# Kernel tuning notes

Measured on AMD Instinct MI355X. Metric: run time of the kernel, lower is better.

## Reference

```python
import jax, jax.numpy as jnp
import numpy as np
from functools import partial

B, T, P, W = 32, 4096, 512, 128
NMEL, FILT, PDIM, K = 80, 256, 64, 9
PAD = (K - 1) // 2  # original uses (kernel[0][0]-1)//2 for both convs
EPS = 1e-5


def setup_inputs() -> dict:
    key = jax.random.key(0)
    ks = jax.random.split(key, 8)
    inp = {}
    inp["mask"] = jnp.zeros((B, P), dtype=bool)
    inp["mels"] = jax.random.normal(ks[0], (B, T, NMEL), dtype=jnp.float32)
    inp["mel_mask"] = jnp.zeros((B, T), dtype=bool)
    # uniform segments: 8 frames per phone (sum == T), 4 phones per word (sum == P)
    inp["durations"] = jnp.full((B, P), T // P, dtype=jnp.int32)
    inp["word_phone_len"] = jnp.full((B, W), P // W, dtype=jnp.int32)
    s1 = 1.0 / np.sqrt(NMEL * K)
    s2 = 1.0 / np.sqrt(FILT * K)
    s3 = 1.0 / np.sqrt(FILT)
    inp["conv1_w"] = jax.random.normal(ks[1], (FILT, NMEL, K), dtype=jnp.float32) * s1
    inp["conv1_b"] = jnp.zeros((FILT,), dtype=jnp.float32)
    inp["ln1_g"] = jnp.ones((FILT,), dtype=jnp.float32)
    inp["ln1_b"] = jnp.zeros((FILT,), dtype=jnp.float32)
    inp["conv2_w"] = jax.random.normal(ks[2], (FILT, FILT, K), dtype=jnp.float32) * s2
    inp["conv2_b"] = jnp.zeros((FILT,), dtype=jnp.float32)
    inp["ln2_g"] = jnp.ones((FILT,), dtype=jnp.float32)
    inp["ln2_b"] = jnp.zeros((FILT,), dtype=jnp.float32)
    inp["w1"] = jax.random.normal(ks[3], (FILT, FILT), dtype=jnp.float32) * s3
    inp["b1"] = jnp.zeros((FILT,), dtype=jnp.float32)
    inp["w2"] = jax.random.normal(ks[4], (FILT, PDIM), dtype=jnp.float32) * s3
    inp["b2"] = jnp.zeros((PDIM,), dtype=jnp.float32)
    return inp


def conv1d(x, w, b):
    # x: [B, T, Cin], w: [Cout, Cin, K] -> [B, T, Cout]
    y = jax.lax.conv_general_dilated(x.transpose(0, 2, 1), w, (1,), [(PAD, PAD)])
    return y.transpose(0, 2, 1) + b


def layernorm(x, g, b):
    m = jnp.mean(x, axis=-1, keepdims=True)
    v = jnp.mean(jnp.square(x - m), axis=-1, keepdims=True)
    return (x - m) * jax.lax.rsqrt(v + EPS) * g + b


def seg_mean(feat, lens, n_seg):
    # feat: [L, D], lens: [S] -> [n_seg, D] segment means
    bounds = jnp.cumsum(lens)
    ids = jnp.searchsorted(bounds, jnp.arange(feat.shape[0]), side="right")
    s = jax.ops.segment_sum(feat, ids, num_segments=n_seg)
    cnt = jnp.maximum(lens, 1).astype(feat.dtype)
    return s / cnt[:, None]


def expand_words(word_emb, wlens, n_out):
    # word_emb: [W, D]; scatter each word embedding across its phones -> [n_out, D]
    bounds = jnp.cumsum(wlens)
    wid = jnp.searchsorted(bounds, jnp.arange(n_out), side="right")
    return word_emb[jnp.clip(wid, 0, word_emb.shape[0] - 1)]


def reference(mask, mels, mel_mask, durations, word_phone_len,
              conv1_w, conv1_b, ln1_g, ln1_b, conv2_w, conv2_b, ln2_g, ln2_b,
              w1, b1, w2, b2):
    x = conv1d(mels, conv1_w, conv1_b)
    x = layernorm(jax.nn.relu(x), ln1_g, ln1_b)
    x = conv1d(x, conv2_w, conv2_b)
    x = layernorm(jax.nn.relu(x), ln2_g, ln2_b)  # [B, T, FILT]
    # token-wise (phone) mean pool over mel frames
    x = jax.vmap(partial(seg_mean, n_seg=P))(x, durations)  # [B, P, FILT]
    # word-level mean pool over phones
    x = jax.vmap(partial(seg_mean, n_seg=W))(x, word_phone_len)  # [B, W, FILT]
    x = jax.nn.relu(x @ w1 + b1)
    x = jax.nn.relu(x @ w2 + b2)  # [B, W, PDIM]
    # expand word embeddings back to phone level
    x = jax.vmap(partial(expand_words, n_out=P))(x, word_phone_len)  # [B, P, PDIM]
    x = jnp.where(mask[..., None], 0.0, x)
    return x
```

## Files before the change

### kernel.cpp

```cpp
#include <hip/hip_runtime.h>
#include <hip/hip_fp16.h>
#include <stdint.h>

#define B_ 32
#define T_ 4096
#define P_ 512
#define W_ 128
#define NMEL 80
#define FILT 256
#define PDIM 64
#define KW 9
#define TP8 (T_ + 8)
#define MSTR 104
#define YSTR 264
#define EPS 1e-5f

typedef unsigned short u16;
typedef __attribute__((ext_vector_type(8))) short short8;
typedef __attribute__((ext_vector_type(4))) float f32x4;

typedef const __attribute__((address_space(1))) uint32_t* gptr_t;
typedef __attribute__((address_space(3))) uint32_t* lptr_t;

__device__ __forceinline__ u16 f2h(float v){ return __half_as_ushort(__float2half(v)); }

#define MFMA16(accv, av, bv) \
  asm volatile("v_mfma_f32_16x16x32_f16 %0, %1, %2, %0" : "+v"(accv) : "v"(av), "v"(bv))

#define STAGE16K(gbase, lbase) { \
    __builtin_amdgcn_global_load_lds((gptr_t)((gbase) + (wave<<10) + (lane<<4)), \
                                     (lptr_t)((lbase) + (wave<<10)), 16, 0, 0); \
    __builtin_amdgcn_global_load_lds((gptr_t)((gbase) + 8192 + (wave<<10) + (lane<<4)), \
                                     (lptr_t)((lbase) + 8192 + (wave<<10)), 16, 0, 0); \
  }

__global__ void pack_w(const float* __restrict__ w1, const float* __restrict__ w2,
                       u16* __restrict__ Wp1, u16* __restrict__ Wp2){
  int i = blockIdx.x * 256 + threadIdx.x;
  const int N1 = KW * 12 * FILT;
  const int N2 = KW * 32 * FILT;
  if (i < N1){
    int tap = i / (12*FILT); int r = i - tap*12*FILT; int kg = r / FILT; int co = r - kg*FILT;
    short8 v;
    #pragma unroll
    for (int e=0;e<8;e++){
      int ci = kg*8 + e;
      float x = (ci < NMEL) ? w1[(co*NMEL + ci)*KW + tap] : 0.f;
      v[e] = (short)f2h(x);
    }
    *(short8*)(Wp1 + (size_t)i*8) = v;
  } else if (i < N1 + N2){
    int j = i - N1;
    int tap = j / (32*FILT); int r = j - tap*32*FILT; int kg = r / FILT; int co = r - kg*FILT;
    short8 v;
    #pragma unroll
    for (int e=0;e<8;e++){
      int ci = kg*8 + e;
      v[e] = (short)f2h(w2[(co*FILT + ci)*KW + tap]);
    }
    *(short8*)(Wp2 + (size_t)j*8) = v;
  }
}

__global__ void prep_mels(const float* __restrict__ mels, u16* __restrict__ melsPad){
  int idx = blockIdx.x * 256 + threadIdx.x;
  if (idx >= B_*TP8*13) return;
  int ch = idx % 13; int r = idx / 13; int row = r % TP8; int b = r / TP8;
  int t = row - 4;
  short8 v = (short8){0,0,0,0,0,0,0,0};
  if (t >= 0 && t < T_ && ch < 10){
    const float* src = mels + ((size_t)b*T_ + t)*NMEL + ch*8;
    const f32x4 f0 = *(const f32x4*)src;
    const f32x4 f1 = *(const f32x4*)(src+4);
    #pragma unroll
    for (int j=0;j<4;j++){ v[j]=(short)f2h(f0[j]); v[4+j]=(short)f2h(f1[j]); }
  }
  *(short8*)(melsPad + (size_t)idx*8) = v;
}

__global__ void prep_seg(const int* __restrict__ dur, const int* __restrict__ wpl,
                         int* __restrict__ wcum,
                         int* __restrict__ pid, int* __restrict__ wid,
                         u16* __restrict__ y1Pad){
  int b = blockIdx.x; int tid = threadIdx.x;
  __shared__ int dc[P_];
  __shared__ int wc[W_];
  for (int p=tid; p<P_; p+=256) dc[p] = dur[b*P_+p];
  if (tid < W_) wc[tid] = wpl[b*W_+tid];
  __syncthreads();
  if (tid == 0){ int run=0; for (int p=0;p<P_;p++){ run += dc[p]; dc[p]=run; } }
  if (tid == 64){ int run=0; for (int w=0;w<W_;w++){ run += wc[w]; wc[w]=run; wcum[b*W_+w]=run; } }
  __syncthreads();
  for (int t=tid; t<T_; t+=256){
    int lo=0, hi=P_;
    while (lo < hi){ int mid=(lo+hi)>>1; if (dc[mid] > t) hi=mid; else lo=mid+1; }
    pid[b*T_+t] = lo;
  }
  for (int p=tid; p<P_; p+=256){
    int lo=0, hi=W_;
    while (lo < hi){ int mid=(lo+hi)>>1; if (wc[mid] > p) hi=mid; else lo=mid+1; }
    wid[b*P_+p] = min(lo, W_-1);
  }
  for (int i=tid; i<8*YSTR; i+=256){
    int rr = i / YSTR; int cc = i - rr*YSTR;
    int row = (rr < 4) ? rr : (T_ + rr);
    y1Pad[((size_t)b*TP8 + row)*YSTR + cc] = 0;
  }
}

__global__ __launch_bounds__(512, 6) void conv1_k(
    const u16* __restrict__ melsPad, const u16* __restrict__ Wp1,
    const float* __restrict__ bias, const float* __restrict__ lng,
    const float* __restrict__ lnb, u16* __restrict__ y1Pad){
  __shared__ __align__(16) u16 sA[8192];
  __shared__ __align__(16) u16 sR[2*8192];
  const int tid = threadIdx.x;
  const int wave = tid >> 6, lane = tid & 63, lo = lane & 15, hi = lane >> 4;
  const int b = blockIdx.y, t0 = blockIdx.x * 64;

  float bcol[2], gcol[2], btcol[2];
  #pragma unroll
  for (int n=0;n<2;n++){
    int c = wave*32 + n*16 + lo;
    bcol[n]=bias[c]; gcol[n]=lng[c]; btcol[n]=lnb[c];
  }

  {
    const char* gA = (const char*)(melsPad + ((size_t)b*TP8 + t0)*MSTR);
    #pragma unroll
    for (int it=0; it<2; ++it)
      __builtin_amdgcn_global_load_lds((gptr_t)(gA + it*8192 + (wave<<10) + (lane<<4)),
                                       (lptr_t)((char*)sA + it*8192 + (wave<<10)), 16, 0, 0);
  }
  const char* gW = (const char*)Wp1;
  char* ring = (char*)sR;
  STAGE16K(gW, ring)
  __syncthreads();

  f32x4 acc[4][2];
  #pragma unroll
  for (int m=0;m<4;m++)
    #pragma unroll
    for (int n=0;n<2;n++) acc[m][n] = (f32x4){0.f,0.f,0.f,0.f};

#define C1_IT(cc, WN) { \
    __builtin_amdgcn_s_barrier(); \
    __builtin_amdgcn_sched_barrier(0); \
    if ((cc)+1 < 27) STAGE16K(gW + (size_t)((cc)+1)*16384, ring + ((((cc)+1)&1)<<14)) \
    asm volatile("s_waitcnt vmcnt(" #WN ")" ::: "memory"); \
    __builtin_amdgcn_sched_barrier(0); \
    const int tap_=(cc)/3, s_=(cc)%3; \
    const u16* bufB = (const u16*)(ring + (((cc)&1)<<14)); \
    short8 av[4], wv[2]; \
    _Pragma("unroll") for (int m=0;m<4;m++) \
      av[m] = *(const short8*)(sA + (m*16 + lo + tap_)*MSTR + s_*32 + hi*8); \
    _Pragma("unroll") for (int n=0;n<2;n++) \
      wv[n] = *(const short8*)(bufB + (hi*256 + wave*32 + n*16 + lo)*8); \
    asm volatile("s_waitcnt lgkmcnt(0)" ::: "memory"); \
    __builtin_amdgcn_sched_barrier(0); \
    __builtin_amdgcn_s_setprio(1); \
    _Pragma("unroll") for (int m=0;m<4;m++) \
      _Pragma("unroll") for (int n=0;n<2;n++) \
        MFMA16(acc[m][n], av[m], wv[n]); \
    __builtin_amdgcn_s_setprio(0); \
  }

  #pragma unroll 1
  for (int cc=0; cc<26; ++cc) C1_IT(cc, 2)
  C1_IT(26, 0)

  asm volatile("s_nop 7\n\ts_nop 7" :: );
  __syncthreads();

  float* sred  = (float*)sR;
  float* sred2 = sred + 512;
  float* smean = sred2 + 512;
  float* srstd = smean + 64;

  #pragma unroll
  for (int m=0;m<4;m++){
    #pragma unroll
    for (int jj=0;jj<4;jj++){
      float s=0.f, q=0.f;
      #pragma unroll
      for (int n=0;n<2;n++){
        float v = fmaxf(acc[m][n][jj] + bcol[n], 0.f);
        s += v; q += v*v;
      }
      #pragma unroll
      for (int off=1; off<16; off<<=1){ s += __shfl_xor(s, off); q += __shfl_xor(q, off); }
      if (lo == 0){ int r = m*16 + hi*4 + jj; sred[r*8+wave] = s; sred2[r*8+wave] = q; }
    }
  }
  __syncthreads();
  if (tid < 64){
    float ss=0.f, qq=0.f;
    #pragma unroll
    for (int w2=0; w2<8; w2++){ ss += sred[tid*8+w2]; qq += sred2[tid*8+w2]; }
    float mean = ss * (1.f/FILT);
    float var  = qq * (1.f/FILT) - mean*mean;
    smean[tid] = mean;
    srstd[tid] = rsqrtf(fmaxf(var, 0.f) + EPS);
  }
  __syncthreads();
  #pragma unroll
  for (int m=0;m<4;m++){
    #pragma unroll
    for (int jj=0;jj<4;jj++){
      int r = m*16 + hi*4 + jj;
      float mn = smean[r], rs = srstd[r];
      #pragma unroll
      for (int n=0;n<2;n++){
        float v = fmaxf(acc[m][n][jj] + bcol[n], 0.f);
        float o = (v - mn)*rs*gcol[n] + btcol[n];
        y1Pad[((size_t)b*TP8 + 4 + t0 + r)*YSTR + wave*32 + n*16 + lo] = f2h(o);
      }
    }
  }
}

__global__ __launch_bounds__(512, 4) void conv2_k(
    const u16* __restrict__ y1Pad, const u16* __restrict__ Wp2,
    const float* __restrict__ bias, const float* __restrict__ lng,
    const float* __restrict__ lnb, const int* __restrict__ pid,
    float* __restrict__ ps){
  __shared__ __align__(16) u16 sA[20480];
  __shared__ __align__(16) u16 sR[2*8192];
  __shared__ int pidT[64];
  const int tid = threadIdx.x;
  const int wave = tid >> 6, lane = tid & 63, lo = lane & 15, hi = lane >> 4;
  const int b = blockIdx.y, t0 = blockIdx.x * 64;

  float bcol[2], gcol[2], btcol[2];
  #pragma unroll
  for (int n=0;n<2;n++){
    int c = wave*32 + n*16 + lo;
    bcol[n]=bias[c]; gcol[n]=lng[c]; btcol[n]=lnb[c];
  }
  if (tid < 64) pidT[tid] = pid[b*T_ + t0 + tid];

  {
    const char* gA = (const char*)(y1Pad + ((size_t)b*TP8 + t0)*YSTR);
    #pragma unroll
    for (int it=0; it<5; ++it)
      __builtin_amdgcn_global_load_lds((gptr_t)(gA + it*8192 + (wave<<10) + (lane<<4)),
                                       (lptr_t)((char*)sA + it*8192 + (wave<<10)), 16, 0, 0);
  }
  const char* gW = (const char*)Wp2;
  char* ring = (char*)sR;
  STAGE16K(gW, ring)
  __syncthreads();

  f32x4 acc[4][2];
  #pragma unroll
  for (int m=0;m<4;m++)
    #pragma unroll
    for (int n=0;n<2;n++) acc[m][n] = (f32x4){0.f,0.f,0.f,0.f};

#define C2_IT(cc, WN) { \
    __builtin_amdgcn_s_barrier(); \
    __builtin_amdgcn_sched_barrier(0); \
    if ((cc)+1 < 72) STAGE16K(gW + (size_t)((cc)+1)*16384, ring + ((((cc)+1)&1)<<14)) \
    asm volatile("s_waitcnt vmcnt(" #WN ")" ::: "memory"); \
    __builtin_amdgcn_sched_barrier(0); \
    const int tap_=(cc)>>3, sg_=(cc)&7; \
    const u16* bufB = (const u16*)(ring + (((cc)&1)<<14)); \
    short8 av[4], wv[2]; \
    _Pragma("unroll") for (int m=0;m<4;m++) \
      av[m] = *(const short8*)(sA + (m*16 + lo + tap_)*YSTR + sg_*32 + hi*8); \
    _Pragma("unroll") for (int n=0;n<2;n++) \
      wv[n] = *(const short8*)(bufB + (hi*256 + wave*32 + n*16 + lo)*8); \
    asm volatile("s_waitcnt lgkmcnt(0)" ::: "memory"); \
    __builtin_amdgcn_sched_barrier(0); \
    __builtin_amdgcn_s_setprio(1); \
    _Pragma("unroll") for (int m=0;m<4;m++) \
      _Pragma("unroll") for (int n=0;n<2;n++) \
        MFMA16(acc[m][n], av[m], wv[n]); \
    __builtin_amdgcn_s_setprio(0); \
  }

  #pragma unroll 1
  for (int cc=0; cc<71; ++cc) C2_IT(cc, 2)
  C2_IT(71, 0)

  asm volatile("s_nop 7\n\ts_nop 7" :: );
  __syncthreads();

  float* sred  = (float*)sR;
  float* sred2 = sred + 512;
  float* smean = sred2 + 512;
  float* srstd = smean + 64;

  #pragma unroll
  for (int m=0;m<4;m++){
    #pragma unroll
    for (int jj=0;jj<4;jj++){
      float s=0.f, q=0.f;
      #pragma unroll
      for (int n=0;n<2;n++){
        float v = fmaxf(acc[m][n][jj] + bcol[n], 0.f);
        s += v; q += v*v;
      }
      #pragma unroll
      for (int off=1; off<16; off<<=1){ s += __shfl_xor(s, off); q += __shfl_xor(q, off); }
      if (lo == 0){ int r = m*16 + hi*4 + jj; sred[r*8+wave] = s; sred2[r*8+wave] = q; }
    }
  }
  __syncthreads();
  if (tid < 64){
    float ss=0.f, qq=0.f;
    #pragma unroll
    for (int w2=0; w2<8; w2++){ ss += sred[tid*8+w2]; qq += sred2[tid*8+w2]; }
    float mean = ss * (1.f/FILT);
    float var  = qq * (1.f/FILT) - mean*mean;
    smean[tid] = mean;
    srstd[tid] = rsqrtf(fmaxf(var, 0.f) + EPS);
  }
  __syncthreads();

  #pragma unroll
  for (int m=0;m<4;m++){
    int rbase = m*16 + hi*4;
    int p0v = pidT[rbase], p3v = pidT[rbase+3];
    int fold = (p0v == p3v);
    float mn[4], rs[4];
    #pragma unroll
    for (int jj=0;jj<4;jj++){ int r = rbase+jj; mn[jj]=smean[r]; rs[jj]=srstd[r]; }
    #pragma unroll
    for (int n=0;n<2;n++){
      int c = wave*32 + n*16 + lo;
      float o[4];
      #pragma unroll
      for (int jj=0;jj<4;jj++){
        float v = fmaxf(acc[m][n][jj] + bcol[n], 0.f);
        o[jj] = (v - mn[jj])*rs[jj]*gcol[n] + btcol[n];
      }
      float s4 = fold ? (o[0]+o[1]+o[2]+o[3]) : 0.f;
      float sp = __shfl_xor(s4, 16);
      int   pp = __shfl_xor(p0v, 16);
      int   fp = __shfl_xor(fold, 16);
      float* base = ps + (size_t)b*P_*FILT;
      if (fold){
        if (p0v < P_){
          if (fp && pp == p0v){
            if ((hi & 1) == 0) atomicAdd(base + (size_t)p0v*FILT + c, s4 + sp);
          } else {
            atomicAdd(base + (size_t)p0v*FILT + c, s4);
          }
        }
      } else {
        #pragma unroll
        for (int jj=0;jj<4;jj++){
          int pj = pidT[rbase+jj];
          if (pj < P_) atomicAdd(base + (size_t)pj*FILT + c, o[jj]);
        }
      }
    }
  }
}

#define WPB 8
__global__ __launch_bounds__(256) void word_k(
    const float* __restrict__ ps, const int* __restrict__ dur,
    const int* __restrict__ wcum, const int* __restrict__ wpl,
    const float* __restrict__ w1, const float* __restrict__ b1,
    const float* __restrict__ w2, const float* __restrict__ b2,
    float* __restrict__ wemb){
  int b = blockIdx.y, wg = blockIdx.x * WPB, tid = threadIdx.x;
  __shared__ float wvS[WPB][FILT];
  __shared__ float h1S[WPB][FILT];
  #pragma unroll
  for (int k=0;k<WPB;k++){
    int w = wg + k;
    int p1 = wcum[b*W_ + w]; int p0 = (w == 0) ? 0 : wcum[b*W_ + w - 1];
    if (p1 > P_) p1 = P_;
    int len = wpl[b*W_ + w];
    float a = 0.f;
    for (int p = p0; p < p1; ++p){
      int d = dur[b*P_ + p]; d = d < 1 ? 1 : d;
      a += ps[((size_t)(b*P_ + p))*FILT + tid] / (float)d;
    }
    wvS[k][tid] = a / (float)(len < 1 ? 1 : len);
  }
  __syncthreads();
  float acc[WPB];
  #pragma unroll
  for (int k=0;k<WPB;k++) acc[k] = b1[tid];
  for (int i=0;i<FILT;i++){
    float wcol = w1[i*FILT + tid];
    #pragma unroll
    for (int k=0;k<WPB;k++) acc[k] += wvS[k][i] * wcol;
  }
  #pragma unroll
  for (int k=0;k<WPB;k++) h1S[k][tid] = fmaxf(acc[k], 0.f);
  __syncthreads();
  int c = tid & 63, kq = tid >> 6;
  #pragma unroll
  for (int kk=kq; kk<WPB; kk+=4){
    float u = b2[c];
    for (int i=0;i<FILT;i++) u += h1S[kk][i] * w2[i*PDIM + c];
    wemb[((size_t)(b*W_ + wg + kk))*PDIM + c] = fmaxf(u, 0.f);
  }
}

__global__ void expand_k(const float* __restrict__ wemb, const int* __restrict__ wid,
                         const unsigned char* __restrict__ mask, float* __restrict__ out){
  int idx = blockIdx.x * 256 + threadIdx.x;
  if (idx >= B_*P_*16) return;
  int q = idx & 15; int p = (idx >> 4) & 511; int bb = idx >> 13;
  int w = wid[bb*P_ + p];
  f32x4 v = *(const f32x4*)(wemb + ((size_t)(bb*W_ + w))*PDIM + q*4);
  if (mask[bb*P_ + p]) v = (f32x4){0.f,0.f,0.f,0.f};
  *(f32x4*)(out + (size_t)idx*4) = v;
}

extern "C" void kernel_launch(void* const* d_in, const int* in_sizes, int n_in,
                              void* d_out, int out_size, void* d_ws, size_t ws_size,
                              hipStream_t stream) {
  const unsigned char* mask = (const unsigned char*)d_in[0];
  const float* mels = (const float*)d_in[1];
  const int*   dur  = (const int*)d_in[3];
  const int*   wpl  = (const int*)d_in[4];
  const float* c1w  = (const float*)d_in[5];
  const float* c1b  = (const float*)d_in[6];
  const float* l1g  = (const float*)d_in[7];
  const float* l1b  = (const float*)d_in[8];
  const float* c2w  = (const float*)d_in[9];
  const float* c2b  = (const float*)d_in[10];
  const float* l2g  = (const float*)d_in[11];
  const float* l2b  = (const float*)d_in[12];
  const float* w1   = (const float*)d_in[13];
  const float* b1   = (const float*)d_in[14];
  const float* w2   = (const float*)d_in[15];
  const float* b2   = (const float*)d_in[16];

  char* ws = (char*)d_ws;
  size_t off = 0;
  auto alloc = [&](size_t bytes){ void* p = ws + off; off += (bytes + 255) & ~(size_t)255; return p; };
  u16* melsPad = (u16*)alloc((size_t)B_*TP8*MSTR*2 + 16384);
  u16* y1Pad   = (u16*)alloc((size_t)B_*TP8*YSTR*2 + 16384);
  u16* Wp1     = (u16*)alloc((size_t)KW*12*FILT*8*2);
  u16* Wp2     = (u16*)alloc((size_t)KW*32*FILT*8*2 + 16384);
  int* wcum    = (int*)alloc((size_t)B_*W_*4);
  int* pid     = (int*)alloc((size_t)B_*T_*4);
  int* wid     = (int*)alloc((size_t)B_*P_*4);
  float* psum  = (float*)alloc((size_t)B_*P_*FILT*4);
  float* wemb  = (float*)alloc((size_t)B_*W_*PDIM*4);

  hipMemsetAsync(psum, 0, (size_t)B_*P_*FILT*4, stream);
  pack_w<<<(KW*12*FILT + KW*32*FILT + 255)/256, 256, 0, stream>>>(c1w, c2w, Wp1, Wp2);
  prep_mels<<<(B_*TP8*13 + 255)/256, 256, 0, stream>>>(mels, melsPad);
  prep_seg<<<B_, 256, 0, stream>>>(dur, wpl, wcum, pid, wid, y1Pad);
  conv1_k<<<dim3(T_/64, B_), 512, 0, stream>>>(melsPad, Wp1, c1b, l1g, l1b, y1Pad);
  conv2_k<<<dim3(T_/64, B_), 512, 0, stream>>>(y1Pad, Wp2, c2b, l2g, l2b, pid, psum);
  word_k<<<dim3(W_/WPB, B_), 256, 0, stream>>>(psum, dur, wcum, wpl, w1, b1, w2, b2, wemb);
  expand_k<<<(B_*P_*16 + 255)/256, 256, 0, stream>>>(wemb, wid, mask, (float*)d_out);
}
```

Before: 382.8 us.

## Retile conv kernels to 128-row blocks with 32x32 MFMA and register-streamed weights

Both convolution kernels now process 128 time rows per block with 4 waves, each wave owning 64 output channels and computing with 32x32x16 MFMA tiles instead of 16x16x32. Weights are no longer staged through an LDS ring with barriers. Each lane loads them directly from global memory into registers and prefetches one chunk ahead, which removes the per-iteration block barrier. The larger per-wave tile is meant to raise MFMA density and weight reuse, at the cost of more accumulator registers and LDS per block, which lowers occupancy. Padding of the workspace buffers is enlarged to cover the bigger input tile loads.

```diff
diff --git a/kernel.cpp b/kernel.cpp
--- a/kernel.cpp
+++ b/kernel.cpp
@@ -18,21 +18,15 @@
 typedef unsigned short u16;
 typedef __attribute__((ext_vector_type(8))) short short8;
 typedef __attribute__((ext_vector_type(4))) float f32x4;
+typedef __attribute__((ext_vector_type(16))) float f32x16;
 
 typedef const __attribute__((address_space(1))) uint32_t* gptr_t;
 typedef __attribute__((address_space(3))) uint32_t* lptr_t;
 
 __device__ __forceinline__ u16 f2h(float v){ return __half_as_ushort(__float2half(v)); }
 
-#define MFMA16(accv, av, bv) \
-  asm volatile("v_mfma_f32_16x16x32_f16 %0, %1, %2, %0" : "+v"(accv) : "v"(av), "v"(bv))
-
-#define STAGE16K(gbase, lbase) { \
-    __builtin_amdgcn_global_load_lds((gptr_t)((gbase) + (wave<<10) + (lane<<4)), \
-                                     (lptr_t)((lbase) + (wave<<10)), 16, 0, 0); \
-    __builtin_amdgcn_global_load_lds((gptr_t)((gbase) + 8192 + (wave<<10) + (lane<<4)), \
-                                     (lptr_t)((lbase) + 8192 + (wave<<10)), 16, 0, 0); \
-  }
+#define MFMA32(accv, av, bv) \
+  asm volatile("v_mfma_f32_32x32x16_f16 %0, %1, %2, %0" : "+v"(accv) : "v"(av), "v"(bv))
 
 __global__ void pack_w(const float* __restrict__ w1, const float* __restrict__ w2,
                        u16* __restrict__ Wp1, u16* __restrict__ Wp2){
@@ -108,209 +102,213 @@
   }
 }
 
-__global__ __launch_bounds__(512, 6) void conv1_k(
+__global__ __launch_bounds__(256, 2) void conv1_k(
     const u16* __restrict__ melsPad, const u16* __restrict__ Wp1,
     const float* __restrict__ bias, const float* __restrict__ lng,
     const float* __restrict__ lnb, u16* __restrict__ y1Pad){
-  __shared__ __align__(16) u16 sA[8192];
-  __shared__ __align__(16) u16 sR[2*8192];
+  __shared__ __align__(16) u16 sA[14144];
+  __shared__ float sred[512], sred2[512], smean[128], srstd[128];
   const int tid = threadIdx.x;
-  const int wave = tid >> 6, lane = tid & 63, lo = lane & 15, hi = lane >> 4;
-  const int b = blockIdx.y, t0 = blockIdx.x * 64;
+  const int cg = tid >> 6, lane = tid & 63, l31 = lane & 31, h = lane >> 5;
+  const int b = blockIdx.y, t0 = blockIdx.x * 128;
 
   float bcol[2], gcol[2], btcol[2];
   #pragma unroll
   for (int n=0;n<2;n++){
-    int c = wave*32 + n*16 + lo;
+    int c = cg*64 + n*32 + l31;
     bcol[n]=bias[c]; gcol[n]=lng[c]; btcol[n]=lnb[c];
   }
 
   {
     const char* gA = (const char*)(melsPad + ((size_t)b*TP8 + t0)*MSTR);
     #pragma unroll
-    for (int it=0; it<2; ++it)
-      __builtin_amdgcn_global_load_lds((gptr_t)(gA + it*8192 + (wave<<10) + (lane<<4)),
-                                       (lptr_t)((char*)sA + it*8192 + (wave<<10)), 16, 0, 0);
-  }
-  const char* gW = (const char*)Wp1;
-  char* ring = (char*)sR;
-  STAGE16K(gW, ring)
-  __syncthreads();
-
-  f32x4 acc[4][2];
-  #pragma unroll
-  for (int m=0;m<4;m++)
-    #pragma unroll
-    for (int n=0;n<2;n++) acc[m][n] = (f32x4){0.f,0.f,0.f,0.f};
-
-#define C1_IT(cc, WN) { \
-    __builtin_amdgcn_s_barrier(); \
-    __builtin_amdgcn_sched_barrier(0); \
-    if ((cc)+1 < 27) STAGE16K(gW + (size_t)((cc)+1)*16384, ring + ((((cc)+1)&1)<<14)) \
-    asm volatile("s_waitcnt vmcnt(" #WN ")" ::: "memory"); \
-    __builtin_amdgcn_sched_barrier(0); \
-    const int tap_=(cc)/3, s_=(cc)%3; \
-    const u16* bufB = (const u16*)(ring + (((cc)&1)<<14)); \
-    short8 av[4], wv[2]; \
-    _Pragma("unroll") for (int m=0;m<4;m++) \
-      av[m] = *(const short8*)(sA + (m*16 + lo + tap_)*MSTR + s_*32 + hi*8); \
-    _Pragma("unroll") for (int n=0;n<2;n++) \
-      wv[n] = *(const short8*)(bufB + (hi*256 + wave*32 + n*16 + lo)*8); \
-    asm volatile("s_waitcnt lgkmcnt(0)" ::: "memory"); \
-    __builtin_amdgcn_sched_barrier(0); \
-    __builtin_amdgcn_s_setprio(1); \
-    _Pragma("unroll") for (int m=0;m<4;m++) \
-      _Pragma("unroll") for (int n=0;n<2;n++) \
-        MFMA16(acc[m][n], av[m], wv[n]); \
-    __builtin_amdgcn_s_setprio(0); \
-  }
-
-  #pragma unroll 1
-  for (int cc=0; cc<26; ++cc) C1_IT(cc, 2)
-  C1_IT(26, 0)
-
-  asm volatile("s_nop 7\n\ts_nop 7" :: );
-  __syncthreads();
-
-  float* sred  = (float*)sR;
-  float* sred2 = sred + 512;
-  float* smean = sred2 + 512;
-  float* srstd = smean + 64;
-
-  #pragma unroll
-  for (int m=0;m<4;m++){
-    #pragma unroll
-    for (int jj=0;jj<4;jj++){
-      float s=0.f, q=0.f;
-      #pragma unroll
-      for (int n=0;n<2;n++){
-        float v = fmaxf(acc[m][n][jj] + bcol[n], 0.f);
-        s += v; q += v*v;
-      }
-      #pragma unroll
-      for (int off=1; off<16; off<<=1){ s += __shfl_xor(s, off); q += __shfl_xor(q, off); }
-      if (lo == 0){ int r = m*16 + hi*4 + jj; sred[r*8+wave] = s; sred2[r*8+wave] = q; }
+    for (int it=0; it<7; ++it)
+      if (it*4096 + tid*16 < 28288)
+        __builtin_amdgcn_global_load_lds((gptr_t)(gA + it*4096 + (cg<<10) + (lane<<4)),
+                                         (lptr_t)((char*)sA + it*4096 + (cg<<10)), 16, 0, 0);
+  }
+
+  const char* gB = (const char*)Wp1 + h*4096 + cg*1024 + (l31<<4);
+#define LOADB1(cc, D) { const char* nb_ = gB + (size_t)(cc)*16384; \
+    D[0][0]=*(const short8*)(nb_);      D[0][1]=*(const short8*)(nb_+512); \
+    D[1][0]=*(const short8*)(nb_+8192); D[1][1]=*(const short8*)(nb_+8704); }
+
+  short8 nb[2][2];
+  LOADB1(0, nb)
+  __syncthreads();
+
+  f32x16 acc[2][2][2] = {};
+
+  #pragma unroll 2
+  for (int cc=0; cc<27; ++cc){
+    short8 bb[2][2];
+    #pragma unroll
+    for (int s2=0;s2<2;++s2)
+      #pragma unroll
+      for (int cb=0;cb<2;++cb) bb[s2][cb] = nb[s2][cb];
+    if (cc+1 < 27) LOADB1(cc+1, nb)
+    const int tap = cc/3, s = cc - tap*3;
+    const u16* pA = sA + (l31 + tap)*MSTR + s*32 + h*8;
+    #pragma unroll
+    for (int st=0; st<2; ++st){
+      short8 a[2][2];
+      #pragma unroll
+      for (int rb=0; rb<2; ++rb)
+        #pragma unroll
+        for (int s2=0; s2<2; ++s2)
+          a[rb][s2] = *(const short8*)(pA + (st*64 + rb*32)*MSTR + s2*16);
+      #pragma unroll
+      for (int rb=0; rb<2; ++rb){
+        MFMA32(acc[st][rb][0], a[rb][0], bb[0][0]);
+        MFMA32(acc[st][rb][0], a[rb][1], bb[1][0]);
+        MFMA32(acc[st][rb][1], a[rb][0], bb[0][1]);
+        MFMA32(acc[st][rb][1], a[rb][1], bb[1][1]);
+      }
     }
   }
-  __syncthreads();
-  if (tid < 64){
+
+  asm volatile("s_nop 7\n\ts_nop 7\n\ts_nop 7" :: );
+
+  #pragma unroll
+  for (int st=0;st<2;++st)
+    #pragma unroll
+    for (int rb=0;rb<2;++rb)
+      #pragma unroll
+      for (int r=0;r<16;++r){
+        float v0 = fmaxf(acc[st][rb][0][r] + bcol[0], 0.f);
+        float v1 = fmaxf(acc[st][rb][1][r] + bcol[1], 0.f);
+        float s = v0+v1, q = v0*v0+v1*v1;
+        #pragma unroll
+        for (int off=1; off<32; off<<=1){ s += __shfl_xor(s, off); q += __shfl_xor(q, off); }
+        if (l31 == 0){ int row = st*64 + rb*32 + (r&3) + 8*(r>>2) + 4*h;
+          sred[row*4+cg]=s; sred2[row*4+cg]=q; }
+      }
+  __syncthreads();
+  if (tid < 128){
     float ss=0.f, qq=0.f;
     #pragma unroll
-    for (int w2=0; w2<8; w2++){ ss += sred[tid*8+w2]; qq += sred2[tid*8+w2]; }
+    for (int w2=0; w2<4; w2++){ ss += sred[tid*4+w2]; qq += sred2[tid*4+w2]; }
     float mean = ss * (1.f/FILT);
     float var  = qq * (1.f/FILT) - mean*mean;
     smean[tid] = mean;
     srstd[tid] = rsqrtf(fmaxf(var, 0.f) + EPS);
   }
   __syncthreads();
-  #pragma unroll
-  for (int m=0;m<4;m++){
-    #pragma unroll
-    for (int jj=0;jj<4;jj++){
-      int r = m*16 + hi*4 + jj;
-      float mn = smean[r], rs = srstd[r];
-      #pragma unroll
-      for (int n=0;n<2;n++){
-        float v = fmaxf(acc[m][n][jj] + bcol[n], 0.f);
-        float o = (v - mn)*rs*gcol[n] + btcol[n];
-        y1Pad[((size_t)b*TP8 + 4 + t0 + r)*YSTR + wave*32 + n*16 + lo] = f2h(o);
-      }
-    }
-  }
-}
-
-__global__ __launch_bounds__(512, 4) void conv2_k(
+
+  #pragma unroll
+  for (int st=0;st<2;++st)
+    #pragma unroll
+    for (int rb=0;rb<2;++rb)
+      #pragma unroll
+      for (int q=0;q<4;++q){
+        const int rbase = st*64 + rb*32 + q*8 + 4*h;
+        float mn0=smean[rbase+0],mn1=smean[rbase+1],mn2=smean[rbase+2],mn3=smean[rbase+3];
+        float rs0=srstd[rbase+0],rs1=srstd[rbase+1],rs2=srstd[rbase+2],rs3=srstd[rbase+3];
+        #pragma unroll
+        for (int cb=0;cb<2;++cb){
+          int c = cg*64 + cb*32 + l31;
+          float x0 = fmaxf(acc[st][rb][cb][q*4+0] + bcol[cb], 0.f);
+          float x1 = fmaxf(acc[st][rb][cb][q*4+1] + bcol[cb], 0.f);
+          float x2 = fmaxf(acc[st][rb][cb][q*4+2] + bcol[cb], 0.f);
+          float x3 = fmaxf(acc[st][rb][cb][q*4+3] + bcol[cb], 0.f);
+          u16* dst = y1Pad + ((size_t)b*TP8 + 4 + t0 + rbase)*YSTR + c;
+          dst[0*YSTR] = f2h((x0-mn0)*rs0*gcol[cb]+btcol[cb]);
+          dst[1*YSTR] = f2h((x1-mn1)*rs1*gcol[cb]+btcol[cb]);
+          dst[2*YSTR] = f2h((x2-mn2)*rs2*gcol[cb]+btcol[cb]);
+          dst[3*YSTR] = f2h((x3-mn3)*rs3*gcol[cb]+btcol[cb]);
+        }
+      }
+}
+
+__global__ __launch_bounds__(256, 2) void conv2_k(
     const u16* __restrict__ y1Pad, const u16* __restrict__ Wp2,
     const float* __restrict__ bias, const float* __restrict__ lng,
     const float* __restrict__ lnb, const int* __restrict__ pid,
     float* __restrict__ ps){
-  __shared__ __align__(16) u16 sA[20480];
-  __shared__ __align__(16) u16 sR[2*8192];
-  __shared__ int pidT[64];
+  __shared__ __align__(16) u16 sA[35904];
+  __shared__ float sred[512], sred2[512], smean[128], srstd[128];
+  __shared__ int pidT[128];
   const int tid = threadIdx.x;
-  const int wave = tid >> 6, lane = tid & 63, lo = lane & 15, hi = lane >> 4;
-  const int b = blockIdx.y, t0 = blockIdx.x * 64;
+  const int cg = tid >> 6, lane = tid & 63, l31 = lane & 31, h = lane >> 5;
+  const int b = blockIdx.y, t0 = blockIdx.x * 128;
 
   float bcol[2], gcol[2], btcol[2];
   #pragma unroll
   for (int n=0;n<2;n++){
-    int c = wave*32 + n*16 + lo;
+    int c = cg*64 + n*32 + l31;
     bcol[n]=bias[c]; gcol[n]=lng[c]; btcol[n]=lnb[c];
   }
-  if (tid < 64) pidT[tid] = pid[b*T_ + t0 + tid];
+  if (tid < 128) pidT[tid] = pid[b*T_ + t0 + tid];
 
   {
     const char* gA = (const char*)(y1Pad + ((size_t)b*TP8 + t0)*YSTR);
     #pragma unroll
-    for (int it=0; it<5; ++it)
-      __builtin_amdgcn_global_load_lds((gptr_t)(gA + it*8192 + (wave<<10) + (lane<<4)),
-                                       (lptr_t)((char*)sA + it*8192 + (wave<<10)), 16, 0, 0);
-  }
-  const char* gW = (const char*)Wp2;
-  char* ring = (char*)sR;
-  STAGE16K(gW, ring)
-  __syncthreads();
-
-  f32x4 acc[4][2];
-  #pragma unroll
-  for (int m=0;m<4;m++)
-    #pragma unroll
-    for (int n=0;n<2;n++) acc[m][n] = (f32x4){0.f,0.f,0.f,0.f};
-
-#define C2_IT(cc, WN) { \
-    __builtin_amdgcn_s_barrier(); \
-    __builtin_amdgcn_sched_barrier(0); \
-    if ((cc)+1 < 72) STAGE16K(gW + (size_t)((cc)+1)*16384, ring + ((((cc)+1)&1)<<14)) \
-    asm volatile("s_waitcnt vmcnt(" #WN ")" ::: "memory"); \
-    __builtin_amdgcn_sched_barrier(0); \
-    const int tap_=(cc)>>3, sg_=(cc)&7; \
-    const u16* bufB = (const u16*)(ring + (((cc)&1)<<14)); \
-    short8 av[4], wv[2]; \
-    _Pragma("unroll") for (int m=0;m<4;m++) \
-      av[m] = *(const short8*)(sA + (m*16 + lo + tap_)*YSTR + sg_*32 + hi*8); \
-    _Pragma("unroll") for (int n=0;n<2;n++) \
-      wv[n] = *(const short8*)(bufB + (hi*256 + wave*32 + n*16 + lo)*8); \
-    asm volatile("s_waitcnt lgkmcnt(0)" ::: "memory"); \
-    __builtin_amdgcn_sched_barrier(0); \
-    __builtin_amdgcn_s_setprio(1); \
-    _Pragma("unroll") for (int m=0;m<4;m++) \
-      _Pragma("unroll") for (int n=0;n<2;n++) \
-        MFMA16(acc[m][n], av[m], wv[n]); \
-    __builtin_amdgcn_s_setprio(0); \
-  }
-
-  #pragma unroll 1
-  for (int cc=0; cc<71; ++cc) C2_IT(cc, 2)
-  C2_IT(71, 0)
-
-  asm volatile("s_nop 7\n\ts_nop 7" :: );
-  __syncthreads();
-
-  float* sred  = (float*)sR;
-  float* sred2 = sred + 512;
-  float* smean = sred2 + 512;
-  float* srstd = smean + 64;
-
-  #pragma unroll
-  for (int m=0;m<4;m++){
-    #pragma unroll
-    for (int jj=0;jj<4;jj++){
-      float s=0.f, q=0.f;
-      #pragma unroll
-      for (int n=0;n<2;n++){
-        float v = fmaxf(acc[m][n][jj] + bcol[n], 0.f);
-        s += v; q += v*v;
-      }
-      #pragma unroll
-      for (int off=1; off<16; off<<=1){ s += __shfl_xor(s, off); q += __shfl_xor(q, off); }
-      if (lo == 0){ int r = m*16 + hi*4 + jj; sred[r*8+wave] = s; sred2[r*8+wave] = q; }
+    for (int it=0; it<18; ++it)
+      if (it*4096 + tid*16 < 71808)
+        __builtin_amdgcn_global_load_lds((gptr_t)(gA + it*4096 + (cg<<10) + (lane<<4)),
+                                         (lptr_t)((char*)sA + it*4096 + (cg<<10)), 16, 0, 0);
+  }
+
+  const char* gB = (const char*)Wp2 + h*4096 + cg*1024 + (l31<<4);
+#define LOADB2(cc, D) { const char* nb_ = gB + (size_t)(cc)*16384; \
+    D[0][0]=*(const short8*)(nb_);      D[0][1]=*(const short8*)(nb_+512); \
+    D[1][0]=*(const short8*)(nb_+8192); D[1][1]=*(const short8*)(nb_+8704); }
+
+  short8 nb[2][2];
+  LOADB2(0, nb)
+  __syncthreads();
+
+  f32x16 acc[2][2][2] = {};
+
+  #pragma unroll 2
+  for (int cc=0; cc<72; ++cc){
+    short8 bb[2][2];
+    #pragma unroll
+    for (int s2=0;s2<2;++s2)
+      #pragma unroll
+      for (int cb=0;cb<2;++cb) bb[s2][cb] = nb[s2][cb];
+    if (cc+1 < 72) LOADB2(cc+1, nb)
+    const int tap = cc>>3, sg = cc&7;
+    const u16* pA = sA + (l31 + tap)*YSTR + sg*32 + h*8;
+    #pragma unroll
+    for (int st=0; st<2; ++st){
+      short8 a[2][2];
+      #pragma unroll
+      for (int rb=0; rb<2; ++rb)
+        #pragma unroll
+        for (int s2=0; s2<2; ++s2)
+          a[rb][s2] = *(const short8*)(pA + (st*64 + rb*32)*YSTR + s2*16);
+      #pragma unroll
+      for (int rb=0; rb<2; ++rb){
+        MFMA32(acc[st][rb][0], a[rb][0], bb[0][0]);
+        MFMA32(acc[st][rb][0], a[rb][1], bb[1][0]);
+        MFMA32(acc[st][rb][1], a[rb][0], bb[0][1]);
+        MFMA32(acc[st][rb][1], a[rb][1], bb[1][1]);
+      }
     }
   }
-  __syncthreads();
-  if (tid < 64){
+
+  asm volatile("s_nop 7\n\ts_nop 7\n\ts_nop 7" :: );
+
+  #pragma unroll
+  for (int st=0;st<2;++st)
+    #pragma unroll
+    for (int rb=0;rb<2;++rb)
+      #pragma unroll
+      for (int r=0;r<16;++r){
+        float v0 = fmaxf(acc[st][rb][0][r] + bcol[0], 0.f);
+        float v1 = fmaxf(acc[st][rb][1][r] + bcol[1], 0.f);
+        float s = v0+v1, q = v0*v0+v1*v1;
+        #pragma unroll
+        for (int off=1; off<32; off<<=1){ s += __shfl_xor(s, off); q += __shfl_xor(q, off); }
+        if (l31 == 0){ int row = st*64 + rb*32 + (r&3) + 8*(r>>2) + 4*h;
+          sred[row*4+cg]=s; sred2[row*4+cg]=q; }
+      }
+  __syncthreads();
+  if (tid < 128){
     float ss=0.f, qq=0.f;
     #pragma unroll
-    for (int w2=0; w2<8; w2++){ ss += sred[tid*8+w2]; qq += sred2[tid*8+w2]; }
+    for (int w2=0; w2<4; w2++){ ss += sred[tid*4+w2]; qq += sred2[tid*4+w2]; }
     float mean = ss * (1.f/FILT);
     float var  = qq * (1.f/FILT) - mean*mean;
     smean[tid] = mean;
@@ -319,44 +317,44 @@
   __syncthreads();
 
   #pragma unroll
-  for (int m=0;m<4;m++){
-    int rbase = m*16 + hi*4;
-    int p0v = pidT[rbase], p3v = pidT[rbase+3];
-    int fold = (p0v == p3v);
-    float mn[4], rs[4];
-    #pragma unroll
-    for (int jj=0;jj<4;jj++){ int r = rbase+jj; mn[jj]=smean[r]; rs[jj]=srstd[r]; }
-    #pragma unroll
-    for (int n=0;n<2;n++){
-      int c = wave*32 + n*16 + lo;
-      float o[4];
-      #pragma unroll
-      for (int jj=0;jj<4;jj++){
-        float v = fmaxf(acc[m][n][jj] + bcol[n], 0.f);
-        o[jj] = (v - mn[jj])*rs[jj]*gcol[n] + btcol[n];
-      }
-      float s4 = fold ? (o[0]+o[1]+o[2]+o[3]) : 0.f;
-      float sp = __shfl_xor(s4, 16);
-      int   pp = __shfl_xor(p0v, 16);
-      int   fp = __shfl_xor(fold, 16);
-      float* base = ps + (size_t)b*P_*FILT;
-      if (fold){
-        if (p0v < P_){
-          if (fp && pp == p0v){
-            if ((hi & 1) == 0) atomicAdd(base + (size_t)p0v*FILT + c, s4 + sp);
+  for (int st=0;st<2;++st)
+    #pragma unroll
+    for (int rb=0;rb<2;++rb)
+      #pragma unroll
+      for (int q=0;q<4;++q){
+        const int rbase = st*64 + rb*32 + q*8 + 4*h;
+        int p0v = pidT[rbase]; int fold = (p0v == pidT[rbase+3]);
+        float mn0=smean[rbase+0],mn1=smean[rbase+1],mn2=smean[rbase+2],mn3=smean[rbase+3];
+        float rs0=srstd[rbase+0],rs1=srstd[rbase+1],rs2=srstd[rbase+2],rs3=srstd[rbase+3];
+        int pp = __shfl_xor(p0v, 32); int fp = __shfl_xor(fold, 32);
+        #pragma unroll
+        for (int cb=0;cb<2;++cb){
+          int c = cg*64 + cb*32 + l31;
+          float x0 = fmaxf(acc[st][rb][cb][q*4+0] + bcol[cb], 0.f);
+          float x1 = fmaxf(acc[st][rb][cb][q*4+1] + bcol[cb], 0.f);
+          float x2 = fmaxf(acc[st][rb][cb][q*4+2] + bcol[cb], 0.f);
+          float x3 = fmaxf(acc[st][rb][cb][q*4+3] + bcol[cb], 0.f);
+          float o0 = (x0-mn0)*rs0*gcol[cb]+btcol[cb];
+          float o1 = (x1-mn1)*rs1*gcol[cb]+btcol[cb];
+          float o2 = (x2-mn2)*rs2*gcol[cb]+btcol[cb];
+          float o3 = (x3-mn3)*rs3*gcol[cb]+btcol[cb];
+          float s4 = fold ? (o0+o1+o2+o3) : 0.f;
+          float sp = __shfl_xor(s4, 32);
+          float* basep = ps + (size_t)b*P_*FILT;
+          if (fold){
+            if (p0v < P_){
+              if (fp && pp == p0v){ if (h == 0) atomicAdd(basep + (size_t)p0v*FILT + c, s4 + sp); }
+              else atomicAdd(basep + (size_t)p0v*FILT + c, s4);
+            }
           } else {
-            atomicAdd(base + (size_t)p0v*FILT + c, s4);
+            int pj;
+            pj = pidT[rbase+0]; if (pj < P_) atomicAdd(basep + (size_t)pj*FILT + c, o0);
+            pj = pidT[rbase+1]; if (pj < P_) atomicAdd(basep + (size_t)pj*FILT + c, o1);
+            pj = pidT[rbase+2]; if (pj < P_) atomicAdd(basep + (size_t)pj*FILT + c, o2);
+            pj = pidT[rbase+3]; if (pj < P_) atomicAdd(basep + (size_t)pj*FILT + c, o3);
           }
         }
-      } else {
-        #pragma unroll
-        for (int jj=0;jj<4;jj++){
-          int pj = pidT[rbase+jj];
-          if (pj < P_) atomicAdd(base + (size_t)pj*FILT + c, o[jj]);
-        }
-      }
-    }
-  }
+      }
 }
 
 #define WPB 8
@@ -437,10 +435,10 @@
   char* ws = (char*)d_ws;
   size_t off = 0;
   auto alloc = [&](size_t bytes){ void* p = ws + off; off += (bytes + 255) & ~(size_t)255; return p; };
-  u16* melsPad = (u16*)alloc((size_t)B_*TP8*MSTR*2 + 16384);
-  u16* y1Pad   = (u16*)alloc((size_t)B_*TP8*YSTR*2 + 16384);
+  u16* melsPad = (u16*)alloc((size_t)B_*TP8*MSTR*2 + 32768);
+  u16* y1Pad   = (u16*)alloc((size_t)B_*TP8*YSTR*2 + 32768);
   u16* Wp1     = (u16*)alloc((size_t)KW*12*FILT*8*2);
-  u16* Wp2     = (u16*)alloc((size_t)KW*32*FILT*8*2 + 16384);
+  u16* Wp2     = (u16*)alloc((size_t)KW*32*FILT*8*2 + 32768);
   int* wcum    = (int*)alloc((size_t)B_*W_*4);
   int* pid     = (int*)alloc((size_t)B_*T_*4);
   int* wid     = (int*)alloc((size_t)B_*P_*4);
@@ -451,8 +449,8 @@
   pack_w<<<(KW*12*FILT + KW*32*FILT + 255)/256, 256, 0, stream>>>(c1w, c2w, Wp1, Wp2);
   prep_mels<<<(B_*TP8*13 + 255)/256, 256, 0, stream>>>(mels, melsPad);
   prep_seg<<<B_, 256, 0, stream>>>(dur, wpl, wcum, pid, wid, y1Pad);
-  conv1_k<<<dim3(T_/64, B_), 512, 0, stream>>>(melsPad, Wp1, c1b, l1g, l1b, y1Pad);
-  conv2_k<<<dim3(T_/64, B_), 512, 0, stream>>>(y1Pad, Wp2, c2b, l2g, l2b, pid, psum);
+  conv1_k<<<dim3(T_/128, B_), 256, 0, stream>>>(melsPad, Wp1, c1b, l1g, l1b, y1Pad);
+  conv2_k<<<dim3(T_/128, B_), 256, 0, stream>>>(y1Pad, Wp2, c2b, l2g, l2b, pid, psum);
   word_k<<<dim3(W_/WPB, B_), 256, 0, stream>>>(psum, dur, wcum, wpl, w1, b1, w2, b2, wemb);
   expand_k<<<(B_*P_*16 + 255)/256, 256, 0, stream>>>(wemb, wid, mask, (float*)d_out);
 }
```

After: 351.9 us. 8.1% less time.
